# Optimization experiments

Measured on AMD Instinct MI355X. Metric: run time of the kernel, lower is better.

## Reference

```python
import jax, jax.numpy as jnp
import numpy as np

N_HEAD, D_MODEL, D_K, D_V = 8, 512, 64, 64
LN_EPS = 1e-3


def setup_inputs() -> dict:
    key = jax.random.key(0)
    ks = jax.random.split(key, 9)
    B, L = 4, 2048
    q = jax.random.normal(ks[0], (B, L, D_MODEL), dtype=jnp.float32)
    k = jax.random.normal(ks[1], (B, L, D_MODEL), dtype=jnp.float32)
    v = jax.random.normal(ks[2], (B, L, D_MODEL), dtype=jnp.float32)
    # xavier-normal-ish init for projections
    s_qk = (2.0 / (D_MODEL + D_K)) ** 0.5
    s_v = (2.0 / (D_MODEL + D_V)) ** 0.5
    s_p = (2.0 / (N_HEAD * D_V + D_MODEL)) ** 0.5
    w_qs = jax.random.normal(ks[3], (N_HEAD, D_MODEL, D_K), dtype=jnp.float32) * s_qk
    w_ks = jax.random.normal(ks[4], (N_HEAD, D_MODEL, D_K), dtype=jnp.float32) * s_qk
    w_vs = jax.random.normal(ks[5], (N_HEAD, D_MODEL, D_V), dtype=jnp.float32) * s_v
    proj_w = jax.random.normal(ks[6], (D_MODEL, N_HEAD * D_V), dtype=jnp.float32) * s_p  # torch Linear weight (out,in)
    proj_b = jnp.zeros((D_MODEL,), dtype=jnp.float32)
    a_2 = jnp.ones((D_MODEL,), dtype=jnp.float32)
    b_2 = jnp.zeros((D_MODEL,), dtype=jnp.float32)
    return {"q": q, "k": k, "v": v, "w_qs": w_qs, "w_ks": w_ks, "w_vs": w_vs,
            "proj_w": proj_w, "proj_b": proj_b, "a_2": a_2, "b_2": b_2}


def _layer_norm(z, a_2, b_2):
    # torch.std default is unbiased (ddof=1); module divides by (sigma + eps)
    mu = jnp.mean(z, axis=-1, keepdims=True)
    sigma = jnp.std(z, axis=-1, keepdims=True, ddof=1)
    return (z - mu) / (sigma + LN_EPS) * a_2 + b_2


def reference(q, k, v, w_qs, w_ks, w_vs, proj_w, proj_b, a_2, b_2):
    B, Lq, D = q.shape
    temper = jnp.asarray(D, q.dtype) ** 0.5  # note: sqrt(d_model), as in source
    residual = q
    # per-head projections: (h, b, l, dk)
    qh = jnp.einsum('bld,hdk->hblk', q, w_qs)
    kh = jnp.einsum('bmd,hdk->hbmk', k, w_ks)
    vh = jnp.einsum('bmd,hdv->hbmv', v, w_vs)
    # full score matrix (h, b, lq, lk) -- faithful to naive bmm attention
    attn = jax.nn.softmax(jnp.einsum('hblk,hbmk->hblm', qh, kh) / temper, axis=-1)
    out = jnp.einsum('hblm,hbmv->hblv', attn, vh)          # (h, b, lq, dv)
    out = jnp.transpose(out, (1, 2, 0, 3)).reshape(B, Lq, -1)  # concat heads -> (b, lq, h*dv)
    out = out @ proj_w.T + proj_b
    out = _layer_norm(out + residual, a_2, b_2)
    attns = attn.reshape(-1, attn.shape[2], attn.shape[3])  # (h*b, lq, lk) matching torch layout
    return out, attns
```

## Files before the change

kernel.cpp:

```cpp
#include <hip/hip_runtime.h>
#include <stdint.h>

typedef unsigned short u16;
typedef u16   u16x4v __attribute__((ext_vector_type(4)));
typedef u16   u16x8v __attribute__((ext_vector_type(8)));
typedef short s16x8v __attribute__((ext_vector_type(8)));
typedef float f32x4v __attribute__((ext_vector_type(4)));

#define DEV static __device__ __forceinline__

DEV u16 f2bf(float f){
  union { float f; unsigned u; } v; v.f = f;
  unsigned r = v.u + 0x7FFFu + ((v.u >> 16) & 1u);
  return (u16)(r >> 16);
}

DEV f32x4v mfma16(s16x8v a, s16x8v b, f32x4v c){
  return __builtin_amdgcn_mfma_f32_16x16x32_bf16(a, b, c, 0, 0, 0);
}

__global__ __launch_bounds__(256) void k_wt(const float* __restrict__ w, u16* __restrict__ wt,
                                            float scale){
  int e = blockIdx.x * 256 + threadIdx.x;
  int n = e >> 9, d = e & 511;
  int h = n >> 6, kk = n & 63;
  wt[e] = f2bf(w[h * 32768 + d * 64 + kk] * scale);
}

__global__ __launch_bounds__(256) void k_wtp(const float* __restrict__ w, u16* __restrict__ wt){
  int e = blockIdx.x * 256 + threadIdx.x;
  wt[e] = f2bf(w[e]);
}

template<int MODE>
__global__ __launch_bounds__(512) void k_proj(const void* __restrict__ Xv,
                                              const u16* __restrict__ Wt,
                                              void* __restrict__ Yv,
                                              const float* __restrict__ bias,
                                              const float* __restrict__ resid,
                                              const float* __restrict__ a2,
                                              const float* __restrict__ b2){
  __shared__ __align__(16) u16 Xs[32 * 520];
  __shared__ float sred[8][32], sqred[8][32], muL[32], rsL[32];
  const int t = threadIdx.x;
  const int lane = t & 63, w = t >> 6;
  const int g = lane >> 4, li = lane & 15;
  const int i0 = blockIdx.x * 32;
  const int n0 = w * 64;

  if(MODE == 2){
    const u16* X = (const u16*)Xv;
    #pragma unroll
    for(int it = 0; it < 4; ++it){
      int s = it * 512 + t, row = s >> 6, c8 = s & 63;
      u16x8v xv = *(const u16x8v*)(X + (size_t)(i0 + row) * 512 + c8 * 8);
      *(u16x8v*)(Xs + row * 520 + c8 * 8) = xv;
    }
  } else {
    const float* X = (const float*)Xv;
    #pragma unroll
    for(int it = 0; it < 8; ++it){
      int s = it * 512 + t, row = s >> 7, c4 = s & 127;
      f32x4v xv = *(const f32x4v*)(X + (size_t)(i0 + row) * 512 + c4 * 4);
      u16x4v bv; bv[0]=f2bf(xv[0]); bv[1]=f2bf(xv[1]); bv[2]=f2bf(xv[2]); bv[3]=f2bf(xv[3]);
      *(u16x4v*)(Xs + row * 520 + c4 * 4) = bv;
    }
  }
  __syncthreads();

  f32x4v acc[2][4] = {};
  #pragma unroll 4
  for(int c = 0; c < 16; ++c){
    int k0 = c * 32 + g * 8;
    s16x8v a0 = *(const s16x8v*)(Xs + li * 520 + k0);
    s16x8v a1 = *(const s16x8v*)(Xs + (16 + li) * 520 + k0);
    #pragma unroll
    for(int j = 0; j < 4; ++j){
      s16x8v b = *(const s16x8v*)(Wt + (size_t)(n0 + j * 16 + li) * 512 + k0);
      acc[0][j] = mfma16(a0, b, acc[0][j]);
      acc[1][j] = mfma16(a1, b, acc[1][j]);
    }
  }

  if(MODE == 0){
    u16* Y = (u16*)Yv;
    #pragma unroll
    for(int qh = 0; qh < 2; ++qh)
      #pragma unroll
      for(int j = 0; j < 4; ++j)
        #pragma unroll
        for(int r = 0; r < 4; ++r){
          int i = i0 + qh * 16 + g * 4 + r, bb = i >> 11, m = i & 2047;
          Y[((size_t)(w * 4 + bb) * 2048 + m) * 64 + j * 16 + li] = f2bf(acc[qh][j][r]);
        }
  } else if(MODE == 1){
    u16* Y = (u16*)Yv;
    #pragma unroll
    for(int qh = 0; qh < 2; ++qh)
      #pragma unroll
      for(int j = 0; j < 4; ++j){
        u16x4v pk;
        #pragma unroll
        for(int r = 0; r < 4; ++r) pk[r] = f2bf(acc[qh][j][r]);
        int n = n0 + j * 16 + li;
        *(u16x4v*)((u16*)Yv + (size_t)n * 8192 + i0 + g * 8 + qh * 4) = pk;
      }
  } else {
    float* Yf = (float*)Yv;
    float biasv[4], a2v[4], b2v[4];
    #pragma unroll
    for(int j = 0; j < 4; ++j){
      int n = n0 + j * 16 + li;
      biasv[j] = bias[n]; a2v[j] = a2[n]; b2v[j] = b2[n];
    }
    float zres[2][4][4];
    #pragma unroll
    for(int qh = 0; qh < 2; ++qh)
      #pragma unroll
      for(int j = 0; j < 4; ++j){
        int n = n0 + j * 16 + li;
        #pragma unroll
        for(int r = 0; r < 4; ++r){
          int i = i0 + qh * 16 + g * 4 + r;
          zres[qh][j][r] = acc[qh][j][r] + biasv[j] + resid[(size_t)i * 512 + n];
        }
      }
    #pragma unroll
    for(int qh = 0; qh < 2; ++qh)
      #pragma unroll
      for(int r = 0; r < 4; ++r){
        float S = 0.f, SQ = 0.f;
        #pragma unroll
        for(int j = 0; j < 4; ++j){ float zz = zres[qh][j][r]; S += zz; SQ += zz * zz; }
        #pragma unroll
        for(int off = 1; off < 16; off <<= 1){ S += __shfl_xor(S, off, 16); SQ += __shfl_xor(SQ, off, 16); }
        if(li == 0){ sred[w][qh * 16 + g * 4 + r] = S; sqred[w][qh * 16 + g * 4 + r] = SQ; }
      }
    __syncthreads();
    if(t < 32){
      float S = 0.f, SQ = 0.f;
      #pragma unroll
      for(int ww = 0; ww < 8; ++ww){ S += sred[ww][t]; SQ += sqred[ww][t]; }
      float mu = S * (1.0f / 512.0f);
      float var = (SQ - 512.0f * mu * mu) * (1.0f / 511.0f);
      muL[t] = mu;
      rsL[t] = 1.0f / (sqrtf(fmaxf(var, 0.0f)) + 1e-3f);
    }
    __syncthreads();
    #pragma unroll
    for(int qh = 0; qh < 2; ++qh)
      #pragma unroll
      for(int r = 0; r < 4; ++r){
        int rloc = qh * 16 + g * 4 + r;
        float mu = muL[rloc], rs = rsL[rloc];
        size_t ib = (size_t)(i0 + rloc) * 512;
        #pragma unroll
        for(int j = 0; j < 4; ++j)
          Yf[ib + n0 + j * 16 + li] = (zres[qh][j][r] - mu) * rs * a2v[j] + b2v[j];
      }
  }
}


#define LOADK(B, ht) { \
  const u16* _p = kp + (size_t)(ht) * 2048; \
  B##0 = *(const s16x8v*)(_p); \
  B##1 = *(const s16x8v*)(_p + 32); \
  B##2 = *(const s16x8v*)(_p + 1024); \
  B##3 = *(const s16x8v*)(_p + 1056); }

#define STEPA(B) { \
  f32x4v z0 = {}, z1 = {}; \
  z0 = mfma16(B##0, bq00, z0); z0 = mfma16(B##1, bq01, z0); \
  z1 = mfma16(B##2, bq00, z1); z1 = mfma16(B##3, bq01, z1); \
  _Pragma("unroll") for(int r = 0; r < 4; ++r){ s00[r] += exp2f(z0[r]); s01[r] += exp2f(z1[r]); } \
  f32x4v y0 = {}, y1 = {}; \
  y0 = mfma16(B##0, bq10, y0); y0 = mfma16(B##1, bq11, y0); \
  y1 = mfma16(B##2, bq10, y1); y1 = mfma16(B##3, bq11, y1); \
  _Pragma("unroll") for(int r = 0; r < 4; ++r){ s10[r] += exp2f(y0[r]); s11[r] += exp2f(y1[r]); } }

#define LOADV(B, ht) { \
  const u16* _p = vp + (ht) * 32; \
  B##0 = *(const s16x8v*)(_p); \
  B##1 = *(const s16x8v*)(_p + 131072); \
  B##2 = *(const s16x8v*)(_p + 262144); \
  B##3 = *(const s16x8v*)(_p + 393216); }

#define QS_HALF(KB, VB, bqa, bqb, rl, qs, ht) { \
  f32x4v z0 = {}, z1 = {}; \
  z0 = mfma16(KB##0, bqa, z0); z0 = mfma16(KB##1, bqb, z0); \
  z1 = mfma16(KB##2, bqa, z1); z1 = mfma16(KB##3, bqb, z1); \
  f32x4v p0, p1; \
  _Pragma("unroll") for(int r = 0; r < 4; ++r){ p0[r] = exp2f(z0[r]) * rl; p1[r] = exp2f(z1[r]) * rl; } \
  float* _ab = attb + (size_t)((qs) * 16 + li) * 2048 + (ht) * 32 + g * 4; \
  __builtin_nontemporal_store(p0, (f32x4v*)(_ab)); \
  __builtin_nontemporal_store(p1, (f32x4v*)(_ab + 16)); \
  union { u16 hh[8]; s16x8v v; } _u; \
  _Pragma("unroll") for(int r = 0; r < 4; ++r){ _u.hh[r] = f2bf(p0[r]); _u.hh[4 + r] = f2bf(p1[r]); } \
  acc##qs##0 = mfma16(_u.v, VB##0, acc##qs##0); \
  acc##qs##1 = mfma16(_u.v, VB##1, acc##qs##1); \
  acc##qs##2 = mfma16(_u.v, VB##2, acc##qs##2); \
  acc##qs##3 = mfma16(_u.v, VB##3, acc##qs##3); }

#define STEPB(KB, VB, ht) { \
  QS_HALF(KB, VB, bq00, bq01, rl0, 0, ht); \
  QS_HALF(KB, VB, bq10, bq11, rl1, 1, ht); }

__global__ __launch_bounds__(256) void k_attn(const u16* __restrict__ QHH, const u16* __restrict__ KHH,
                                              const u16* __restrict__ VTT,
                                              u16* __restrict__ XC, float* __restrict__ ATT){
  const int t = threadIdx.x, lane = t & 63, w = t >> 6;
  const int g = lane >> 4, li = lane & 15;
  const int gid = blockIdx.x;
  const int xcd = gid & 7, rem = gid >> 3;
  const int lt = rem & 15;
  const int hb = xcd * 4 + (rem >> 4);
  const int h = hb >> 2, b = hb & 3;
  const size_t base_hb = (size_t)hb * 2048;
  const int qbase = lt * 128 + w * 32;

  s16x8v bq00, bq01, bq10, bq11;
  {
    const u16* qp0 = QHH + (base_hb + qbase + li) * 64 + g * 8;
    const u16* qp1 = QHH + (base_hb + qbase + 16 + li) * 64 + g * 8;
    bq00 = *(const s16x8v*)(qp0); bq01 = *(const s16x8v*)(qp0 + 32);
    bq10 = *(const s16x8v*)(qp1); bq11 = *(const s16x8v*)(qp1 + 32);
  }
  const u16* kp = KHH + (base_hb + li) * 64 + g * 8;
  const u16* vp = VTT + (size_t)(h * 64 + li) * 8192 + b * 2048 + g * 8;

  f32x4v s00 = {}, s01 = {}, s10 = {}, s11 = {};
  {
    s16x8v kA0, kA1, kA2, kA3, kB0, kB1, kB2, kB3;
    LOADK(kA, 0);
    for(int ht = 0; ht < 62; ht += 2){
      LOADK(kB, ht + 1);
      STEPA(kA);
      LOADK(kA, ht + 2);
      STEPA(kB);
    }
    LOADK(kB, 63);
    STEPA(kA);
    STEPA(kB);
  }
  float l0 = (s00[0]+s00[1]+s00[2]+s00[3]) + (s01[0]+s01[1]+s01[2]+s01[3]);
  float l1 = (s10[0]+s10[1]+s10[2]+s10[3]) + (s11[0]+s11[1]+s11[2]+s11[3]);
  l0 += __shfl_xor(l0, 16, 64); l0 += __shfl_xor(l0, 32, 64);
  l1 += __shfl_xor(l1, 16, 64); l1 += __shfl_xor(l1, 32, 64);
  const float rl0 = 1.0f / l0;
  const float rl1 = 1.0f / l1;

  float* attb = ATT + (base_hb + qbase) * 2048;
  f32x4v acc00 = {}, acc01 = {}, acc02 = {}, acc03 = {};
  f32x4v acc10 = {}, acc11 = {}, acc12 = {}, acc13 = {};
  {
    s16x8v kA0, kA1, kA2, kA3, kB0, kB1, kB2, kB3;
    s16x8v vA0, vA1, vA2, vA3, vB0, vB1, vB2, vB3;
    LOADK(kA, 0); LOADV(vA, 0);
    for(int ht = 0; ht < 62; ht += 2){
      LOADK(kB, ht + 1); LOADV(vB, ht + 1);
      STEPB(kA, vA, ht);
      LOADK(kA, ht + 2); LOADV(vA, ht + 2);
      STEPB(kB, vB, ht + 1);
    }
    LOADK(kB, 63); LOADV(vB, 63);
    STEPB(kA, vA, 62);
    STEPB(kB, vB, 63);
  }

  #pragma unroll
  for(int r = 0; r < 4; ++r){
    int row0 = qbase + g * 4 + r;
    int row1 = qbase + 16 + g * 4 + r;
    u16* x0 = XC + (size_t)(b * 2048 + row0) * 512 + h * 64 + li;
    u16* x1 = XC + (size_t)(b * 2048 + row1) * 512 + h * 64 + li;
    x0[0]  = f2bf(acc00[r]); x0[16] = f2bf(acc01[r]); x0[32] = f2bf(acc02[r]); x0[48] = f2bf(acc03[r]);
    x1[0]  = f2bf(acc10[r]); x1[16] = f2bf(acc11[r]); x1[32] = f2bf(acc12[r]); x1[48] = f2bf(acc13[r]);
  }
}

extern "C" void kernel_launch(void* const* d_in, const int* in_sizes, int n_in,
                              void* d_out, int out_size, void* d_ws, size_t ws_size,
                              hipStream_t stream){
  const float* q      = (const float*)d_in[0];
  const float* k      = (const float*)d_in[1];
  const float* v      = (const float*)d_in[2];
  const float* w_qs   = (const float*)d_in[3];
  const float* w_ks   = (const float*)d_in[4];
  const float* w_vs   = (const float*)d_in[5];
  const float* proj_w = (const float*)d_in[6];
  const float* proj_b = (const float*)d_in[7];
  const float* a2     = (const float*)d_in[8];
  const float* b2     = (const float*)d_in[9];

  char* ws = (char*)d_ws;
  u16* wt    = (u16*)(ws);
  u16* wtp   = (u16*)(ws + 1572864);
  u16* qhh   = (u16*)(ws + 2097152);
  u16* khh   = (u16*)(ws + 10485760);
  u16* vtt   = (u16*)(ws + 18874368);
  u16* xc    = (u16*)(ws + 27262976);

  float* out = (float*)d_out;
  float* att = out + 4194304;

  const float qscale = 0.06375872032774575f;

  k_wt <<<dim3(1024), 256, 0, stream>>>(w_qs, wt,          qscale);
  k_wt <<<dim3(1024), 256, 0, stream>>>(w_ks, wt + 262144, 1.0f);
  k_wt <<<dim3(1024), 256, 0, stream>>>(w_vs, wt + 524288, 1.0f);
  k_wtp<<<dim3(1024), 256, 0, stream>>>(proj_w, wtp);

  k_proj<0><<<dim3(256), 512, 0, stream>>>(q, wt,          qhh, nullptr, nullptr, nullptr, nullptr);
  k_proj<0><<<dim3(256), 512, 0, stream>>>(k, wt + 262144, khh, nullptr, nullptr, nullptr, nullptr);
  k_proj<1><<<dim3(256), 512, 0, stream>>>(v, wt + 524288, vtt, nullptr, nullptr, nullptr, nullptr);

  k_attn<<<dim3(512), 256, 0, stream>>>(qhh, khh, vtt, xc, att);

  k_proj<2><<<dim3(256), 512, 0, stream>>>(xc, wtp, out, proj_b, q, a2, b2);
}
```

Baseline: 323.7 us.

## Merge weight-convert and QKV projection launches, add register prefetch, shrink out-proj tiles

The four weight-conversion kernels become one launch, and the three Q/K/V projection launches become a single 2D grid. That grid has 6x256 blocks of 256 threads, each covering half the output columns. Both the projection and the output kernels now double-buffer weight fragments in registers, so global loads overlap the MFMAs. The output-projection+LayerNorm kernel uses 16-row tiles across 512 blocks to raise occupancy. The aim is to cut launch overhead and raise parallelism in the non-attention stages. The cost is that each X tile is converted twice across the column halves, and more weight traffic is spread over blocks.

```diff
diff --git a/kernel.cpp b/kernel.cpp
--- a/kernel.cpp
+++ b/kernel.cpp
@@ -19,144 +19,107 @@
   return __builtin_amdgcn_mfma_f32_16x16x32_bf16(a, b, c, 0, 0, 0);
 }
 
-__global__ __launch_bounds__(256) void k_wt(const float* __restrict__ w, u16* __restrict__ wt,
-                                            float scale){
-  int e = blockIdx.x * 256 + threadIdx.x;
-  int n = e >> 9, d = e & 511;
-  int h = n >> 6, kk = n & 63;
-  wt[e] = f2bf(w[h * 32768 + d * 64 + kk] * scale);
-}
-
-__global__ __launch_bounds__(256) void k_wtp(const float* __restrict__ w, u16* __restrict__ wt){
-  int e = blockIdx.x * 256 + threadIdx.x;
-  wt[e] = f2bf(w[e]);
-}
-
-template<int MODE>
-__global__ __launch_bounds__(512) void k_proj(const void* __restrict__ Xv,
-                                              const u16* __restrict__ Wt,
-                                              void* __restrict__ Yv,
-                                              const float* __restrict__ bias,
-                                              const float* __restrict__ resid,
-                                              const float* __restrict__ a2,
-                                              const float* __restrict__ b2){
+__global__ __launch_bounds__(256) void k_wall(const float* __restrict__ w_qs,
+                                              const float* __restrict__ w_ks,
+                                              const float* __restrict__ w_vs,
+                                              const float* __restrict__ proj_w,
+                                              u16* __restrict__ wt, u16* __restrict__ wtp,
+                                              float qscale){
+  int gid = blockIdx.x;
+  int tsel = gid >> 10;
+  int e = (gid & 1023) * 256 + threadIdx.x;
+  if(tsel == 3){
+    wtp[e] = f2bf(proj_w[e]);
+  } else {
+    const float* w = tsel == 0 ? w_qs : (tsel == 1 ? w_ks : w_vs);
+    float sc = tsel == 0 ? qscale : 1.0f;
+    int n = e >> 9, d = e & 511;
+    int h = n >> 6, kk = n & 63;
+    wt[tsel * 262144 + n * 512 + d] = f2bf(w[h * 32768 + d * 64 + kk] * sc);
+  }
+}
+
+__global__ __launch_bounds__(256) void k_qkv(const float* __restrict__ Q,
+                                             const float* __restrict__ K,
+                                             const float* __restrict__ V,
+                                             const u16* __restrict__ Wt,
+                                             u16* __restrict__ qhh, u16* __restrict__ khh,
+                                             u16* __restrict__ vtt){
   __shared__ __align__(16) u16 Xs[32 * 520];
-  __shared__ float sred[8][32], sqred[8][32], muL[32], rsL[32];
   const int t = threadIdx.x;
   const int lane = t & 63, w = t >> 6;
   const int g = lane >> 4, li = lane & 15;
   const int i0 = blockIdx.x * 32;
-  const int n0 = w * 64;
-
-  if(MODE == 2){
-    const u16* X = (const u16*)Xv;
-    #pragma unroll
-    for(int it = 0; it < 4; ++it){
-      int s = it * 512 + t, row = s >> 6, c8 = s & 63;
-      u16x8v xv = *(const u16x8v*)(X + (size_t)(i0 + row) * 512 + c8 * 8);
-      *(u16x8v*)(Xs + row * 520 + c8 * 8) = xv;
-    }
-  } else {
-    const float* X = (const float*)Xv;
-    #pragma unroll
-    for(int it = 0; it < 8; ++it){
-      int s = it * 512 + t, row = s >> 7, c4 = s & 127;
-      f32x4v xv = *(const f32x4v*)(X + (size_t)(i0 + row) * 512 + c4 * 4);
-      u16x4v bv; bv[0]=f2bf(xv[0]); bv[1]=f2bf(xv[1]); bv[2]=f2bf(xv[2]); bv[3]=f2bf(xv[3]);
-      *(u16x4v*)(Xs + row * 520 + c4 * 4) = bv;
-    }
+  const int y = blockIdx.y;
+  const int tsel = y >> 1;
+  const float* X = tsel == 0 ? Q : (tsel == 1 ? K : V);
+  const int n0 = (y & 1) * 256 + w * 64;
+
+  #pragma unroll
+  for(int it = 0; it < 16; ++it){
+    int s = it * 256 + t, row = s >> 7, c4 = s & 127;
+    f32x4v xv = *(const f32x4v*)(X + (size_t)(i0 + row) * 512 + c4 * 4);
+    u16x4v bv; bv[0]=f2bf(xv[0]); bv[1]=f2bf(xv[1]); bv[2]=f2bf(xv[2]); bv[3]=f2bf(xv[3]);
+    *(u16x4v*)(Xs + row * 520 + c4 * 4) = bv;
   }
   __syncthreads();
 
+  const int wbase = tsel * 512 + n0;
+  const u16* wp0 = Wt + (size_t)(wbase +  0 + li) * 512 + g * 8;
+  const u16* wp1 = Wt + (size_t)(wbase + 16 + li) * 512 + g * 8;
+  const u16* wp2 = Wt + (size_t)(wbase + 32 + li) * 512 + g * 8;
+  const u16* wp3 = Wt + (size_t)(wbase + 48 + li) * 512 + g * 8;
+
+#define LOADW(S, c) { \
+  S##0 = *(const s16x8v*)(wp0 + (c) * 32); \
+  S##1 = *(const s16x8v*)(wp1 + (c) * 32); \
+  S##2 = *(const s16x8v*)(wp2 + (c) * 32); \
+  S##3 = *(const s16x8v*)(wp3 + (c) * 32); }
+#define COMPW(S, c) { \
+  int k0 = (c) * 32 + g * 8; \
+  s16x8v a0 = *(const s16x8v*)(Xs + li * 520 + k0); \
+  s16x8v a1 = *(const s16x8v*)(Xs + (16 + li) * 520 + k0); \
+  acc[0][0] = mfma16(a0, S##0, acc[0][0]); acc[1][0] = mfma16(a1, S##0, acc[1][0]); \
+  acc[0][1] = mfma16(a0, S##1, acc[0][1]); acc[1][1] = mfma16(a1, S##1, acc[1][1]); \
+  acc[0][2] = mfma16(a0, S##2, acc[0][2]); acc[1][2] = mfma16(a1, S##2, acc[1][2]); \
+  acc[0][3] = mfma16(a0, S##3, acc[0][3]); acc[1][3] = mfma16(a1, S##3, acc[1][3]); }
+
   f32x4v acc[2][4] = {};
-  #pragma unroll 4
-  for(int c = 0; c < 16; ++c){
-    int k0 = c * 32 + g * 8;
-    s16x8v a0 = *(const s16x8v*)(Xs + li * 520 + k0);
-    s16x8v a1 = *(const s16x8v*)(Xs + (16 + li) * 520 + k0);
-    #pragma unroll
-    for(int j = 0; j < 4; ++j){
-      s16x8v b = *(const s16x8v*)(Wt + (size_t)(n0 + j * 16 + li) * 512 + k0);
-      acc[0][j] = mfma16(a0, b, acc[0][j]);
-      acc[1][j] = mfma16(a1, b, acc[1][j]);
-    }
-  }
-
-  if(MODE == 0){
-    u16* Y = (u16*)Yv;
-    #pragma unroll
-    for(int qh = 0; qh < 2; ++qh)
+  s16x8v wA0, wA1, wA2, wA3, wB0, wB1, wB2, wB3;
+  LOADW(wA, 0);
+  #pragma unroll
+  for(int c = 0; c < 16; c += 2){
+    LOADW(wB, c + 1);
+    COMPW(wA, c);
+    if(c + 2 < 16) LOADW(wA, c + 2);
+    COMPW(wB, c + 1);
+  }
+#undef LOADW
+#undef COMPW
+
+  if(tsel < 2){
+    u16* Y = tsel == 0 ? qhh : khh;
+    #pragma unroll
+    for(int rg = 0; rg < 2; ++rg)
       #pragma unroll
-      for(int j = 0; j < 4; ++j)
+      for(int j = 0; j < 4; ++j){
+        int n = n0 + j * 16 + li, h = n >> 6, dk = n & 63;
         #pragma unroll
         for(int r = 0; r < 4; ++r){
-          int i = i0 + qh * 16 + g * 4 + r, bb = i >> 11, m = i & 2047;
-          Y[((size_t)(w * 4 + bb) * 2048 + m) * 64 + j * 16 + li] = f2bf(acc[qh][j][r]);
+          int i = i0 + rg * 16 + g * 4 + r, bb = i >> 11, m = i & 2047;
+          Y[((size_t)(h * 4 + bb) * 2048 + m) * 64 + dk] = f2bf(acc[rg][j][r]);
         }
-  } else if(MODE == 1){
-    u16* Y = (u16*)Yv;
-    #pragma unroll
-    for(int qh = 0; qh < 2; ++qh)
-      #pragma unroll
-      for(int j = 0; j < 4; ++j){
-        u16x4v pk;
-        #pragma unroll
-        for(int r = 0; r < 4; ++r) pk[r] = f2bf(acc[qh][j][r]);
-        int n = n0 + j * 16 + li;
-        *(u16x4v*)((u16*)Yv + (size_t)n * 8192 + i0 + g * 8 + qh * 4) = pk;
       }
   } else {
-    float* Yf = (float*)Yv;
-    float biasv[4], a2v[4], b2v[4];
-    #pragma unroll
-    for(int j = 0; j < 4; ++j){
-      int n = n0 + j * 16 + li;
-      biasv[j] = bias[n]; a2v[j] = a2[n]; b2v[j] = b2[n];
-    }
-    float zres[2][4][4];
-    #pragma unroll
-    for(int qh = 0; qh < 2; ++qh)
+    #pragma unroll
+    for(int rg = 0; rg < 2; ++rg)
       #pragma unroll
       for(int j = 0; j < 4; ++j){
         int n = n0 + j * 16 + li;
+        u16x4v pk;
         #pragma unroll
-        for(int r = 0; r < 4; ++r){
-          int i = i0 + qh * 16 + g * 4 + r;
-          zres[qh][j][r] = acc[qh][j][r] + biasv[j] + resid[(size_t)i * 512 + n];
-        }
-      }
-    #pragma unroll
-    for(int qh = 0; qh < 2; ++qh)
-      #pragma unroll
-      for(int r = 0; r < 4; ++r){
-        float S = 0.f, SQ = 0.f;
-        #pragma unroll
-        for(int j = 0; j < 4; ++j){ float zz = zres[qh][j][r]; S += zz; SQ += zz * zz; }
-        #pragma unroll
-        for(int off = 1; off < 16; off <<= 1){ S += __shfl_xor(S, off, 16); SQ += __shfl_xor(SQ, off, 16); }
-        if(li == 0){ sred[w][qh * 16 + g * 4 + r] = S; sqred[w][qh * 16 + g * 4 + r] = SQ; }
-      }
-    __syncthreads();
-    if(t < 32){
-      float S = 0.f, SQ = 0.f;
-      #pragma unroll
-      for(int ww = 0; ww < 8; ++ww){ S += sred[ww][t]; SQ += sqred[ww][t]; }
-      float mu = S * (1.0f / 512.0f);
-      float var = (SQ - 512.0f * mu * mu) * (1.0f / 511.0f);
-      muL[t] = mu;
-      rsL[t] = 1.0f / (sqrtf(fmaxf(var, 0.0f)) + 1e-3f);
-    }
-    __syncthreads();
-    #pragma unroll
-    for(int qh = 0; qh < 2; ++qh)
-      #pragma unroll
-      for(int r = 0; r < 4; ++r){
-        int rloc = qh * 16 + g * 4 + r;
-        float mu = muL[rloc], rs = rsL[rloc];
-        size_t ib = (size_t)(i0 + rloc) * 512;
-        #pragma unroll
-        for(int j = 0; j < 4; ++j)
-          Yf[ib + n0 + j * 16 + li] = (zres[qh][j][r] - mu) * rs * a2v[j] + b2v[j];
+        for(int r = 0; r < 4; ++r) pk[r] = f2bf(acc[rg][j][r]);
+        *(u16x4v*)(vtt + (size_t)n * 8192 + i0 + g * 8 + rg * 4) = pk;
       }
   }
 }
@@ -279,6 +242,104 @@
   }
 }
 
+__global__ __launch_bounds__(512) void k_out(const u16* __restrict__ Xb,
+                                             const u16* __restrict__ Wtp,
+                                             float* __restrict__ Yf,
+                                             const float* __restrict__ bias,
+                                             const float* __restrict__ resid,
+                                             const float* __restrict__ a2,
+                                             const float* __restrict__ b2){
+  __shared__ __align__(16) u16 Xs[16 * 520];
+  __shared__ float sred[8][16], sqred[8][16], muL[16], rsL[16];
+  const int t = threadIdx.x;
+  const int lane = t & 63, w = t >> 6;
+  const int g = lane >> 4, li = lane & 15;
+  const int i0 = blockIdx.x * 16;
+  const int n0 = w * 64;
+
+  #pragma unroll
+  for(int it = 0; it < 2; ++it){
+    int s = it * 512 + t, row = s >> 6, c8 = s & 63;
+    u16x8v xv = *(const u16x8v*)(Xb + (size_t)(i0 + row) * 512 + c8 * 8);
+    *(u16x8v*)(Xs + row * 520 + c8 * 8) = xv;
+  }
+  __syncthreads();
+
+  const u16* wp0 = Wtp + (size_t)(n0 +  0 + li) * 512 + g * 8;
+  const u16* wp1 = Wtp + (size_t)(n0 + 16 + li) * 512 + g * 8;
+  const u16* wp2 = Wtp + (size_t)(n0 + 32 + li) * 512 + g * 8;
+  const u16* wp3 = Wtp + (size_t)(n0 + 48 + li) * 512 + g * 8;
+
+#define LOADW(S, c) { \
+  S##0 = *(const s16x8v*)(wp0 + (c) * 32); \
+  S##1 = *(const s16x8v*)(wp1 + (c) * 32); \
+  S##2 = *(const s16x8v*)(wp2 + (c) * 32); \
+  S##3 = *(const s16x8v*)(wp3 + (c) * 32); }
+#define COMPW(S, c) { \
+  int k0 = (c) * 32 + g * 8; \
+  s16x8v a0 = *(const s16x8v*)(Xs + li * 520 + k0); \
+  acc[0] = mfma16(a0, S##0, acc[0]); \
+  acc[1] = mfma16(a0, S##1, acc[1]); \
+  acc[2] = mfma16(a0, S##2, acc[2]); \
+  acc[3] = mfma16(a0, S##3, acc[3]); }
+
+  f32x4v acc[4] = {};
+  s16x8v wA0, wA1, wA2, wA3, wB0, wB1, wB2, wB3;
+  LOADW(wA, 0);
+  #pragma unroll
+  for(int c = 0; c < 16; c += 2){
+    LOADW(wB, c + 1);
+    COMPW(wA, c);
+    if(c + 2 < 16) LOADW(wA, c + 2);
+    COMPW(wB, c + 1);
+  }
+#undef LOADW
+#undef COMPW
+
+  float zres[4][4];
+  #pragma unroll
+  for(int j = 0; j < 4; ++j){
+    int n = n0 + j * 16 + li;
+    float bv = bias[n];
+    #pragma unroll
+    for(int r = 0; r < 4; ++r){
+      int i = i0 + g * 4 + r;
+      zres[j][r] = acc[j][r] + bv + resid[(size_t)i * 512 + n];
+    }
+  }
+  #pragma unroll
+  for(int r = 0; r < 4; ++r){
+    float S = 0.f, SQ = 0.f;
+    #pragma unroll
+    for(int j = 0; j < 4; ++j){ float zz = zres[j][r]; S += zz; SQ += zz * zz; }
+    #pragma unroll
+    for(int off = 1; off < 16; off <<= 1){ S += __shfl_xor(S, off, 16); SQ += __shfl_xor(SQ, off, 16); }
+    if(li == 0){ sred[w][g * 4 + r] = S; sqred[w][g * 4 + r] = SQ; }
+  }
+  __syncthreads();
+  if(t < 16){
+    float S = 0.f, SQ = 0.f;
+    #pragma unroll
+    for(int ww = 0; ww < 8; ++ww){ S += sred[ww][t]; SQ += sqred[ww][t]; }
+    float mu = S * (1.0f / 512.0f);
+    float var = (SQ - 512.0f * mu * mu) * (1.0f / 511.0f);
+    muL[t] = mu;
+    rsL[t] = 1.0f / (sqrtf(fmaxf(var, 0.0f)) + 1e-3f);
+  }
+  __syncthreads();
+  #pragma unroll
+  for(int r = 0; r < 4; ++r){
+    int rloc = g * 4 + r;
+    float mu = muL[rloc], rs = rsL[rloc];
+    size_t ib = (size_t)(i0 + rloc) * 512;
+    #pragma unroll
+    for(int j = 0; j < 4; ++j){
+      int n = n0 + j * 16 + li;
+      Yf[ib + n] = (zres[j][r] - mu) * rs * a2[n] + b2[n];
+    }
+  }
+}
+
 extern "C" void kernel_launch(void* const* d_in, const int* in_sizes, int n_in,
                               void* d_out, int out_size, void* d_ws, size_t ws_size,
                               hipStream_t stream){
@@ -306,16 +367,8 @@
 
   const float qscale = 0.06375872032774575f;
 
-  k_wt <<<dim3(1024), 256, 0, stream>>>(w_qs, wt,          qscale);
-  k_wt <<<dim3(1024), 256, 0, stream>>>(w_ks, wt + 262144, 1.0f);
-  k_wt <<<dim3(1024), 256, 0, stream>>>(w_vs, wt + 524288, 1.0f);
-  k_wtp<<<dim3(1024), 256, 0, stream>>>(proj_w, wtp);
-
-  k_proj<0><<<dim3(256), 512, 0, stream>>>(q, wt,          qhh, nullptr, nullptr, nullptr, nullptr);
-  k_proj<0><<<dim3(256), 512, 0, stream>>>(k, wt + 262144, khh, nullptr, nullptr, nullptr, nullptr);
-  k_proj<1><<<dim3(256), 512, 0, stream>>>(v, wt + 524288, vtt, nullptr, nullptr, nullptr, nullptr);
-
+  k_wall<<<dim3(4096), 256, 0, stream>>>(w_qs, w_ks, w_vs, proj_w, wt, wtp, qscale);
+  k_qkv <<<dim3(256, 6), 256, 0, stream>>>(q, k, v, wt, qhh, khh, vtt);
   k_attn<<<dim3(512), 256, 0, stream>>>(qhh, khh, vtt, xc, att);
-
-  k_proj<2><<<dim3(256), 512, 0, stream>>>(xc, wtp, out, proj_b, q, a2, b2);
-}
+  k_out <<<dim3(512), 512, 0, stream>>>(xc, wtp, out, proj_b, q, a2, b2);
+}
```

Result: no change. 318.7 us (-1.5%).
